# Kernel tuning notes

Measured on AMD Instinct MI355X. Metric: run time of the kernel, lower is better.

Reference implementation:

```python
import jax, jax.numpy as jnp
import numpy as np

BS, QLEN, KLEN = 2, 64, 64
N_HEADS, D_KV = 8, 64
INNER = N_HEADS * D_KV  # 512
VOCAB = 4096


def _layernorm(x, g, b, eps=1e-6):
    m = jnp.mean(x, axis=-1, keepdims=True)
    v = jnp.mean(jnp.square(x - m), axis=-1, keepdims=True)
    return (x - m) * jax.lax.rsqrt(v + eps) * g + b


def _l2norm(x, eps=1e-12):
    sq = jnp.sum(jnp.square(x), axis=-1, keepdims=True)
    return x * jax.lax.rsqrt(jnp.maximum(sq, eps))


def setup_inputs() -> dict:
    key = jax.random.key(0)
    ks = jax.random.split(key, 8)
    d = {
        'query': jax.random.normal(ks[0], (BS, QLEN, INNER), jnp.float32),
        'key': jax.random.normal(ks[1], (BS, KLEN, INNER), jnp.float32),
        'q_position_embeddings': jax.random.normal(ks[2], (BS, QLEN, INNER), jnp.float32),
        'k_position_embeddings': jax.random.normal(ks[3], (BS, KLEN, INNER), jnp.float32),
        'wi_w': jax.random.normal(ks[4], (2 * INNER, INNER), jnp.float32) / np.sqrt(2 * INNER),
        'vq_dict': jax.random.normal(ks[5], (VOCAB, D_KV), jnp.float32) * np.sqrt(2.0 / (VOCAB + D_KV)),
        'vq_ln_g': jnp.ones((D_KV,), jnp.float32),
        'vq_ln_b': jnp.zeros((D_KV,), jnp.float32),
        'vq_o_w': jax.random.normal(ks[6], (D_KV, D_KV), jnp.float32) / np.sqrt(D_KV),
        'ln_g': jnp.ones((D_KV,), jnp.float32),
        'ln_b': jnp.zeros((D_KV,), jnp.float32),
    }
    return d


def reference(query, key, q_position_embeddings, k_position_embeddings,
              wi_w, vq_dict, vq_ln_g, vq_ln_b, vq_o_w, ln_g, ln_b):
    bs, qlen, dim = query.shape
    klen = key.shape[1]

    q = query + q_position_embeddings
    k = key + k_position_embeddings
    # wi(concat([q, 0])) == q @ wi_w[:dim]; wi(concat([0, k])) == k @ wi_w[dim:]
    q_proj = jnp.einsum('bqd,de->bqe', q, wi_w[:dim])   # [bs, qlen, inner]
    k_proj = jnp.einsum('bkd,de->bke', k, wi_w[dim:])   # [bs, klen, inner]

    # pairwise outer sum -> [bs, qlen, klen, inner] -> tokens of size d_kv
    rcr = q_proj[:, :, None, :] + k_proj[:, None, :, :]
    y = rcr.reshape(bs, qlen * klen * N_HEADS, D_KV)

    # --- VectorQuantizer (eval mode: no dropout, loss = 0) ---
    y_n = _l2norm(y)
    d_n = _l2norm(vq_dict)
    sim = jnp.einsum('bnd,vd->bnv', y_n, d_n)           # [bs, N, vocab]
    word_idx = jnp.argmax(sim, axis=-1)                 # [bs, N] int
    word_sim = jnp.max(sim, axis=-1)                    # [bs, N]
    z = vq_dict[word_idx]                               # gather
    emb = jax.lax.stop_gradient(z - y) + y              # straight-through
    emb = _layernorm(emb, vq_ln_g, vq_ln_b)
    emb = jnp.einsum('bnd,de->bne', emb, vq_o_w)

    r3 = emb.reshape(bs, qlen, klen, N_HEADS, D_KV)
    r3_scores = word_sim.reshape(bs, qlen, klen, N_HEADS, 1)
    out_ids = word_idx.reshape(bs, qlen, klen, N_HEADS, 1)

    r3_weighted = jnp.mean(r3 * r3_scores, axis=2)      # [bs, qlen, n_heads, d_kv]
    r3_weighted = jnp.transpose(r3_weighted, (0, 2, 1, 3))  # [bs, n_heads, qlen, d_kv]
    r3_weighted = _layernorm(r3_weighted, ln_g, ln_b)
    return r3_weighted, out_ids, r3_scores
```

## Files before the change

kernel.cpp:

```cpp
#include <hip/hip_runtime.h>
#include <math.h>

#define BS 2
#define QLEN 64
#define KLEN 64
#define NH 8
#define DKV 64
#define INNER 512
#define VOCAB 4096
#define CHUNKV 64
#define RS 130
#define BUFD (CHUNKV * RS)

typedef double vdbl4 __attribute__((ext_vector_type(4)));
typedef double vdbl2 __attribute__((ext_vector_type(2)));


__global__ __launch_bounds__(256) void k_prep(
    const float* __restrict__ q_in, const float* __restrict__ k_in,
    const float* __restrict__ qpe, const float* __restrict__ kpe,
    const float* __restrict__ wi,
    const float* __restrict__ vq, const float* __restrict__ g,
    const float* __restrict__ bta, const float* __restrict__ ow,
    double* __restrict__ qp, double* __restrict__ kp,
    double* __restrict__ dnt, float* __restrict__ E,
    unsigned long long* __restrict__ bestf)
{
    __shared__ double S[1600];
    __shared__ float Osh[4096];
    int bid = blockIdx.x;
    int t = threadIdx.x;

    if (bid < 1024) {
        int side = bid >> 9;
        int b    = (bid >> 8) & 1;
        int rp   = (bid >> 3) & 31;
        int cb   = bid & 7;
        const float* xin = side ? k_in : q_in;
        const float* pin = side ? kpe : qpe;
        double* outp = side ? kp : qp;
        int wrow0 = side ? INNER : 0;
        int r0 = rp * 2;
        double* xs = S;
        double* red = S + 1024;
        for (int i = t; i < 2 * INNER; i += 256) {
            int rr = i >> 9, dd = i & 511;
            int gidx = (b * 64 + r0 + rr) * INNER + dd;
            xs[rr * INNER + dd] = (double)xin[gidx] + (double)pin[gidx];
        }
        __syncthreads();
        int col = cb * 64 + (t & 63);
        int dh = t >> 6;
        double a0 = 0.0, a1 = 0.0;
        #pragma unroll 8
        for (int d = dh * 128; d < dh * 128 + 128; ++d) {
            double w = (double)wi[(size_t)(wrow0 + d) * INNER + col];
            a0 = fma(xs[d], w, a0);
            a1 = fma(xs[INNER + d], w, a1);
        }
        red[(dh * 2 + 0) * 64 + (t & 63)] = a0;
        red[(dh * 2 + 1) * 64 + (t & 63)] = a1;
        __syncthreads();
        if (t < 128) {
            int rr = t >> 6, c2 = t & 63;
            double s = (red[(0 * 2 + rr) * 64 + c2] + red[(1 * 2 + rr) * 64 + c2])
                     + (red[(2 * 2 + rr) * 64 + c2] + red[(3 * 2 + rr) * 64 + c2]);
            outp[(size_t)(b * 64 + r0 + rr) * INNER + cb * 64 + c2] = s;
        }
    } else {
        int db = bid - 1024;
        if (db < 256) bestf[db * 256 + t] = 0ull;
        double* Lsh = S;
        double* Dsh = S + 256;
        int vb = db * 4;
        int wv = t >> 6, lane = t & 63;
        for (int i = t; i < 4096; i += 256) Osh[i] = ow[i];
        int v = vb + wv;
        double z = (double)vq[v * DKV + lane];
        double s2 = z * z, s1 = z;
        for (int m = 32; m >= 1; m >>= 1) { s2 += __shfl_xor(s2, m); s1 += __shfl_xor(s1, m); }
        Dsh[lane * 5 + wv] = z * (1.0 / sqrt(fmax(s2, 1e-12)));
        double mean = s1 * (1.0 / 64.0);
        double d0 = z - mean;
        double vv2 = d0 * d0;
        for (int m = 32; m >= 1; m >>= 1) vv2 += __shfl_xor(vv2, m);
        vv2 *= (1.0 / 64.0);
        Lsh[wv * 64 + lane] = d0 * (1.0 / sqrt(vv2 + 1e-6)) * (double)g[lane] + (double)bta[lane];
        __syncthreads();
        double c0 = 0.0, c1 = 0.0, c2 = 0.0, c3 = 0.0;
        #pragma unroll 4
        for (int gg = 0; gg < 16; ++gg) {
            int jj = gg * 4;
            c0 = fma(Lsh[wv * 64 + jj + 0], (double)Osh[(jj + 0) * 64 + lane], c0);
            c1 = fma(Lsh[wv * 64 + jj + 1], (double)Osh[(jj + 1) * 64 + lane], c1);
            c2 = fma(Lsh[wv * 64 + jj + 2], (double)Osh[(jj + 2) * 64 + lane], c2);
            c3 = fma(Lsh[wv * 64 + jj + 3], (double)Osh[(jj + 3) * 64 + lane], c3);
        }
        E[v * DKV + lane] = (float)((c0 + c1) + (c2 + c3));
        {
            int j = t >> 2, vloc = t & 3;
            dnt[(size_t)j * VOCAB + vb + vloc] = Dsh[j * 5 + vloc];
        }
    }
}

__global__ __launch_bounds__(1024, 4) void k_simscan(
    const double* __restrict__ qp, const double* __restrict__ kp,
    const double* __restrict__ dnt,
    unsigned long long* __restrict__ bestf)
{
    int bid = blockIdx.x;
    int bh = bid & 15, cg = bid >> 4;
    int b = bh >> 3, h = bh & 7;
    int t = threadIdx.x;
    int w = t >> 6, l = t & 63;

    __shared__ double S[2 * BUFD];

    int asub = l >> 4;
    int lrow = l & 15;
    bool isprod = (w < 8);

    int drow[4], dcol[4];
    {
        vdbl4 prow = (vdbl4){0.0, 0.0, 0.0, 0.0};
        vdbl4 pcol = (vdbl4){0.0, 0.0, 0.0, 0.0};
        double a_row = (asub == 0) ? (double)lrow : 0.0;
        double b_one = (asub == 0) ? 1.0 : 0.0;
        double a_one = (asub == 0) ? 1.0 : 0.0;
        double b_col = (asub == 0) ? (double)lrow : 0.0;
        prow = __builtin_amdgcn_mfma_f64_16x16x4f64(a_row, b_one, prow, 0, 0, 0);
        pcol = __builtin_amdgcn_mfma_f64_16x16x4f64(a_one, b_col, pcol, 0, 0, 0);
        #pragma unroll
        for (int r = 0; r < 4; ++r) { drow[r] = (int)prow[r]; dcol[r] = (int)pcol[r]; }
    }

    double afr[16];
    if (isprod) {
        const double* src = (w < 4) ? qp : kp;
        int arow = (w & 3) * 16 + lrow;
        #pragma unroll
        for (int ks = 0; ks < 16; ++ks)
            afr[ks] = src[(size_t)(b * 64 + arow) * INNER + h * 64 + ks * 4 + asub];
    }

    int ci = t - 512;
    int qg = ci & 15, kg = (ci >> 4) & 31;
    double best[4][2];
    #pragma unroll
    for (int i = 0; i < 4; ++i)
        #pragma unroll
        for (int j = 0; j < 2; ++j) best[i][j] = 0.0;

    for (int step = 0; step < 5; ++step) {
        if (isprod && step < 4) {
            int v0 = (cg * 4 + step) * CHUNKV;
            double* buf = S + (step & 1) * BUFD;
            vdbl4 acc[4];
            #pragma unroll
            for (int vt = 0; vt < 4; ++vt) acc[vt] = (vdbl4){0.0, 0.0, 0.0, 0.0};
            size_t base = (size_t)asub * VOCAB + v0 + lrow;
            double bcur[4], bnext[4];
            #pragma unroll
            for (int vt = 0; vt < 4; ++vt) bcur[vt] = dnt[base + vt * 16];
            #pragma unroll
            for (int ks = 0; ks < 16; ++ks) {
                if (ks < 15) {
                    size_t krow = base + (size_t)((ks + 1) * 4) * VOCAB;
                    #pragma unroll
                    for (int vt = 0; vt < 4; ++vt) bnext[vt] = dnt[krow + vt * 16];
                }
                #pragma unroll
                for (int vt = 0; vt < 4; ++vt)
                    acc[vt] = __builtin_amdgcn_mfma_f64_16x16x4f64(
                        afr[ks], bcur[vt], acc[vt], 0, 0, 0);
                if (ks < 15) {
                    #pragma unroll
                    for (int vt = 0; vt < 4; ++vt) bcur[vt] = bnext[vt];
                }
            }
            bool isq = (w < 4);
            #pragma unroll
            for (int vt = 0; vt < 4; ++vt)
                #pragma unroll
                for (int r = 0; r < 4; ++r) {
                    int vl = vt * 16 + dcol[r];
                    int grow = (w & 3) * 16 + drow[r];
                    int slot = isq ? ((grow & 15) * 4 + (grow >> 4))
                                   : (64 + (grow & 31) * 2 + (grow >> 5));
                    unsigned long long code =
                        (unsigned long long)((4095 - (v0 + vl)) << 1);
                    double s = fma(acc[vt][r], 1.0 / 64.0, 1.5);
                    unsigned long long bb2 = __double_as_longlong(s) & ~0x1FFFull;
                    if (isq) bb2 |= code;
                    buf[vl * RS + slot] = __longlong_as_double(bb2);
                }
        }
        if (!isprod && step >= 1) {
            double* buf = S + ((step - 1) & 1) * BUFD;
            #pragma unroll 2
            for (int v = 0; v < CHUNKV; ++v) {
                vdbl2 q01 = *(const vdbl2*)&buf[v * RS + qg * 4];
                vdbl2 q23 = *(const vdbl2*)&buf[v * RS + qg * 4 + 2];
                vdbl2 k01 = *(const vdbl2*)&buf[v * RS + 64 + kg * 2];
                best[0][0] = fmax(best[0][0], q01[0] + k01[0]);
                best[0][1] = fmax(best[0][1], q01[0] + k01[1]);
                best[1][0] = fmax(best[1][0], q01[1] + k01[0]);
                best[1][1] = fmax(best[1][1], q01[1] + k01[1]);
                best[2][0] = fmax(best[2][0], q23[0] + k01[0]);
                best[2][1] = fmax(best[2][1], q23[0] + k01[1]);
                best[3][0] = fmax(best[3][0], q23[1] + k01[0]);
                best[3][1] = fmax(best[3][1], q23[1] + k01[1]);
            }
        }
        if (step < 4) __syncthreads();
    }

    if (!isprod) {
        #pragma unroll
        for (int i = 0; i < 4; ++i)
            #pragma unroll
            for (int j = 0; j < 2; ++j) {
                int q = qg + 16 * i, k = kg + 32 * j;
                atomicMax(&bestf[((size_t)bh * 64 + q) * 64 + k],
                          (unsigned long long)__double_as_longlong(best[i][j]));
            }
    }
}

__global__ __launch_bounds__(256) void k_combine(
    const unsigned long long* __restrict__ bestf,
    const double* __restrict__ qp, const double* __restrict__ kp,
    const float* __restrict__ E,
    const float* __restrict__ lng, const float* __restrict__ lnb,
    float* __restrict__ out)
{
    int bid = blockIdx.x;
    int bh = bid >> 4, qg = bid & 15;
    int b = bh >> 3, h = bh & 7;
    int t = threadIdx.x;
    int w = t >> 6, lane = t & 63;
    int q0 = qg * 4;

    __shared__ double SC[4416];
    double* qs_l = SC;
    double* ks_l = SC + 256;
    __shared__ float ws_l[4][64];
    __shared__ int  idx_l[4][64];

    {
        int row = t >> 6, d = t & 63;
        qs_l[row * 64 + d] = qp[(size_t)(b * 64 + q0 + row) * INNER + h * 64 + d];
    }
    for (int i = t; i < 4096; i += 256) {
        int kr = i >> 6, d = i & 63;
        ks_l[kr * 65 + d] = kp[(size_t)(b * 64 + kr) * INNER + h * 64 + d];
    }
    __syncthreads();

    int qq = t >> 6;
    int k = t & 63;
    int q = q0 + qq;
    double gdot = 0.0, qn2 = 0.0, kn2 = 0.0;
    for (int d = 0; d < 64; ++d) {
        double xq = qs_l[qq * 64 + d];
        double xk = ks_l[k * 65 + d];
        gdot = fma(xq, xk, gdot);
        qn2 = fma(xq, xq, qn2);
        kn2 = fma(xk, xk, kn2);
    }

    unsigned long long bb = bestf[((size_t)bh * 64 + q) * 64 + k];
    int vidx = 4095 - (int)(bb & 0xFFFull);
    double sval = __longlong_as_double(bb & ~0x1FFFull);
    double tru = (sval - 3.0) * 64.0;
    double n2 = qn2 + kn2 + 2.0 * gdot;
    double wsim = tru * (1.0 / sqrt(fmax(n2, 1e-12)));

    size_t oidx = ((size_t)(b * QLEN + q) * KLEN + k) * NH + h;
    out[65536 + oidx] = (float)vidx;
    out[131072 + oidx] = (float)wsim;

    ws_l[w][k] = (float)wsim;
    idx_l[w][k] = vidx;
    __syncthreads();

    int d = lane;
    float acc = 0.0f;
    for (int k2 = 0; k2 < 64; ++k2)
        acc += E[idx_l[w][k2] * DKV + d] * ws_l[w][k2];
    acc *= (1.0f / 64.0f);
    float mean = acc;
    for (int m = 32; m >= 1; m >>= 1) mean += __shfl_xor(mean, m);
    mean *= (1.0f / 64.0f);
    float dv = acc - mean;
    float var = dv * dv;
    for (int m = 32; m >= 1; m >>= 1) var += __shfl_xor(var, m);
    var *= (1.0f / 64.0f);
    float o = dv * rsqrtf(var + 1e-6f) * lng[d] + lnb[d];
    out[(((size_t)b * NH + h) * QLEN + q) * DKV + d] = o;
}

extern "C" void kernel_launch(void* const* d_in, const int* in_sizes, int n_in,
                              void* d_out, int out_size, void* d_ws, size_t ws_size,
                              hipStream_t stream) {
    const float* query = (const float*)d_in[0];
    const float* key   = (const float*)d_in[1];
    const float* qpe   = (const float*)d_in[2];
    const float* kpe   = (const float*)d_in[3];
    const float* wi    = (const float*)d_in[4];
    const float* vq    = (const float*)d_in[5];
    const float* vqg   = (const float*)d_in[6];
    const float* vqb   = (const float*)d_in[7];
    const float* ow    = (const float*)d_in[8];
    const float* lng   = (const float*)d_in[9];
    const float* lnb   = (const float*)d_in[10];
    float* out = (float*)d_out;

    char* ws = (char*)d_ws;
    double* qp  = (double*)(ws + 0);
    double* kp  = (double*)(ws + 524288);
    double* dnt = (double*)(ws + 1048576);
    float*  E   = (float*) (ws + 3145728);
    unsigned long long* bestf = (unsigned long long*)(ws + 4194304);

    k_prep   <<<2048, 256, 0, stream>>>(query, key, qpe, kpe, wi, vq, vqg, vqb, ow,
                                        qp, kp, dnt, E, bestf);
    k_simscan<<<256, 1024, 0, stream>>>(qp, kp, dnt, bestf);
    k_combine<<<256, 256, 0, stream>>>(bestf, qp, kp, E, lng, lnb, out);
}
```

Before: 154.9 us.

## Halve simscan block size with 4x4 register tiles and smaller vocab chunks

Restructures the similarity-scan kernel into 512-thread blocks over 32-entry vocab chunks. Each of the four producer waves now computes 2x2 MFMA tiles, reusing each B fragment across two A row tiles. Each consumer thread keeps a 4x4 best tile, giving more reuse per shared-memory load. The grid doubles to 512 blocks to cover the vocabulary, which raises parallelism but also doubles the atomicMax traffic and the redundant A-fragment loads.

```diff
diff --git a/kernel.cpp b/kernel.cpp
--- a/kernel.cpp
+++ b/kernel.cpp
@@ -8,12 +8,11 @@
 #define DKV 64
 #define INNER 512
 #define VOCAB 4096
-#define CHUNKV 64
-#define RS 130
+#define CHUNKV 32
+#define RS 129
 #define BUFD (CHUNKV * RS)
 
 typedef double vdbl4 __attribute__((ext_vector_type(4)));
-typedef double vdbl2 __attribute__((ext_vector_type(2)));
 
 
 __global__ __launch_bounds__(256) void k_prep(
@@ -104,13 +103,13 @@
     }
 }
 
-__global__ __launch_bounds__(1024, 4) void k_simscan(
+__global__ __launch_bounds__(512, 4) void k_simscan(
     const double* __restrict__ qp, const double* __restrict__ kp,
     const double* __restrict__ dnt,
     unsigned long long* __restrict__ bestf)
 {
     int bid = blockIdx.x;
-    int bh = bid & 15, cg = bid >> 4;
+    int bh = bid & 15, vg = bid >> 4;
     int b = bh >> 3, h = bh & 7;
     int t = threadIdx.x;
     int w = t >> 6, l = t & 63;
@@ -119,7 +118,7 @@
 
     int asub = l >> 4;
     int lrow = l & 15;
-    bool isprod = (w < 8);
+    bool isprod = (w < 4);
 
     int drow[4], dcol[4];
     {
@@ -135,82 +134,89 @@
         for (int r = 0; r < 4; ++r) { drow[r] = (int)prow[r]; dcol[r] = (int)pcol[r]; }
     }
 
-    double afr[16];
+    double afr[2][16];
     if (isprod) {
-        const double* src = (w < 4) ? qp : kp;
-        int arow = (w & 3) * 16 + lrow;
+        const double* src = (w < 2) ? qp : kp;
+        int half = w & 1;
         #pragma unroll
-        for (int ks = 0; ks < 16; ++ks)
-            afr[ks] = src[(size_t)(b * 64 + arow) * INNER + h * 64 + ks * 4 + asub];
-    }
-
-    int ci = t - 512;
-    int qg = ci & 15, kg = (ci >> 4) & 31;
-    double best[4][2];
+        for (int rt = 0; rt < 2; ++rt) {
+            int arow = half * 32 + rt * 16 + lrow;
+            #pragma unroll
+            for (int ks = 0; ks < 16; ++ks)
+                afr[rt][ks] = src[(size_t)(b * 64 + arow) * INNER + h * 64 + ks * 4 + asub];
+        }
+    }
+
+    int ci = t - 256;
+    int qg = ci & 15, kg = (ci >> 4) & 15;
+    double best[4][4];
     #pragma unroll
     for (int i = 0; i < 4; ++i)
         #pragma unroll
-        for (int j = 0; j < 2; ++j) best[i][j] = 0.0;
+        for (int j = 0; j < 4; ++j) best[i][j] = 0.0;
 
     for (int step = 0; step < 5; ++step) {
         if (isprod && step < 4) {
-            int v0 = (cg * 4 + step) * CHUNKV;
+            int v0 = (vg * 4 + step) * CHUNKV;
             double* buf = S + (step & 1) * BUFD;
-            vdbl4 acc[4];
-            #pragma unroll
-            for (int vt = 0; vt < 4; ++vt) acc[vt] = (vdbl4){0.0, 0.0, 0.0, 0.0};
+            vdbl4 acc[2][2];
+            #pragma unroll
+            for (int rt = 0; rt < 2; ++rt)
+                #pragma unroll
+                for (int vt = 0; vt < 2; ++vt) acc[rt][vt] = (vdbl4){0.0, 0.0, 0.0, 0.0};
             size_t base = (size_t)asub * VOCAB + v0 + lrow;
-            double bcur[4], bnext[4];
-            #pragma unroll
-            for (int vt = 0; vt < 4; ++vt) bcur[vt] = dnt[base + vt * 16];
+            double bcur[2], bnext[2];
+            #pragma unroll
+            for (int vt = 0; vt < 2; ++vt) bcur[vt] = dnt[base + vt * 16];
             #pragma unroll
             for (int ks = 0; ks < 16; ++ks) {
                 if (ks < 15) {
                     size_t krow = base + (size_t)((ks + 1) * 4) * VOCAB;
                     #pragma unroll
-                    for (int vt = 0; vt < 4; ++vt) bnext[vt] = dnt[krow + vt * 16];
+                    for (int vt = 0; vt < 2; ++vt) bnext[vt] = dnt[krow + vt * 16];
                 }
                 #pragma unroll
-                for (int vt = 0; vt < 4; ++vt)
-                    acc[vt] = __builtin_amdgcn_mfma_f64_16x16x4f64(
-                        afr[ks], bcur[vt], acc[vt], 0, 0, 0);
+                for (int rt = 0; rt < 2; ++rt)
+                    #pragma unroll
+                    for (int vt = 0; vt < 2; ++vt)
+                        acc[rt][vt] = __builtin_amdgcn_mfma_f64_16x16x4f64(
+                            afr[rt][ks], bcur[vt], acc[rt][vt], 0, 0, 0);
                 if (ks < 15) {
                     #pragma unroll
-                    for (int vt = 0; vt < 4; ++vt) bcur[vt] = bnext[vt];
+                    for (int vt = 0; vt < 2; ++vt) bcur[vt] = bnext[vt];
                 }
             }
-            bool isq = (w < 4);
-            #pragma unroll
-            for (int vt = 0; vt < 4; ++vt)
-                #pragma unroll
-                for (int r = 0; r < 4; ++r) {
-                    int vl = vt * 16 + dcol[r];
-                    int grow = (w & 3) * 16 + drow[r];
-                    int slot = isq ? ((grow & 15) * 4 + (grow >> 4))
-                                   : (64 + (grow & 31) * 2 + (grow >> 5));
-                    unsigned long long code =
-                        (unsigned long long)((4095 - (v0 + vl)) << 1);
-                    double s = fma(acc[vt][r], 1.0 / 64.0, 1.5);
-                    unsigned long long bb2 = __double_as_longlong(s) & ~0x1FFFull;
-                    if (isq) bb2 |= code;
-                    buf[vl * RS + slot] = __longlong_as_double(bb2);
-                }
+            bool isq = (w < 2);
+            int rb0 = (isq ? 0 : 64) + (w & 1) * 32;
+            #pragma unroll
+            for (int rt = 0; rt < 2; ++rt)
+                #pragma unroll
+                for (int vt = 0; vt < 2; ++vt)
+                    #pragma unroll
+                    for (int r = 0; r < 4; ++r) {
+                        int vl = vt * 16 + dcol[r];
+                        unsigned long long code =
+                            (unsigned long long)((4095 - (v0 + vl)) << 1);
+                        double s = fma(acc[rt][vt][r], 1.0 / 64.0, 1.5);
+                        unsigned long long bb2 = __double_as_longlong(s) & ~0x1FFFull;
+                        if (isq) bb2 |= code;
+                        buf[vl * RS + rb0 + rt * 16 + drow[r]] = __longlong_as_double(bb2);
+                    }
         }
         if (!isprod && step >= 1) {
             double* buf = S + ((step - 1) & 1) * BUFD;
             #pragma unroll 2
             for (int v = 0; v < CHUNKV; ++v) {
-                vdbl2 q01 = *(const vdbl2*)&buf[v * RS + qg * 4];
-                vdbl2 q23 = *(const vdbl2*)&buf[v * RS + qg * 4 + 2];
-                vdbl2 k01 = *(const vdbl2*)&buf[v * RS + 64 + kg * 2];
-                best[0][0] = fmax(best[0][0], q01[0] + k01[0]);
-                best[0][1] = fmax(best[0][1], q01[0] + k01[1]);
-                best[1][0] = fmax(best[1][0], q01[1] + k01[0]);
-                best[1][1] = fmax(best[1][1], q01[1] + k01[1]);
-                best[2][0] = fmax(best[2][0], q23[0] + k01[0]);
-                best[2][1] = fmax(best[2][1], q23[0] + k01[1]);
-                best[3][0] = fmax(best[3][0], q23[1] + k01[0]);
-                best[3][1] = fmax(best[3][1], q23[1] + k01[1]);
+                double qv[4], kv[4];
+                #pragma unroll
+                for (int i = 0; i < 4; ++i) qv[i] = buf[v * RS + qg + 16 * i];
+                #pragma unroll
+                for (int j = 0; j < 4; ++j) kv[j] = buf[v * RS + 64 + kg + 16 * j];
+                #pragma unroll
+                for (int i = 0; i < 4; ++i)
+                    #pragma unroll
+                    for (int j = 0; j < 4; ++j)
+                        best[i][j] = fmax(best[i][j], qv[i] + kv[j]);
             }
         }
         if (step < 4) __syncthreads();
@@ -220,8 +226,8 @@
         #pragma unroll
         for (int i = 0; i < 4; ++i)
             #pragma unroll
-            for (int j = 0; j < 2; ++j) {
-                int q = qg + 16 * i, k = kg + 32 * j;
+            for (int j = 0; j < 4; ++j) {
+                int q = qg + 16 * i, k = kg + 16 * j;
                 atomicMax(&bestf[((size_t)bh * 64 + q) * 64 + k],
                           (unsigned long long)__double_as_longlong(best[i][j]));
             }
@@ -326,6 +332,6 @@
 
     k_prep   <<<2048, 256, 0, stream>>>(query, key, qpe, kpe, wi, vq, vqg, vqb, ow,
                                         qp, kp, dnt, E, bestf);
-    k_simscan<<<256, 1024, 0, stream>>>(qp, kp, dnt, bestf);
+    k_simscan<<<512, 512, 0, stream>>>(qp, kp, dnt, bestf);
     k_combine<<<256, 256, 0, stream>>>(bestf, qp, kp, E, lng, lnb, out);
 }
```

After: 169.2 us. 9.3% more time.

## Split combine kernel per query row with four-way reductions across waves

Applied to the files above, without the earlier changes.

The combine kernel now runs one block per (batch, head, query) instead of per four queries, giving 1024 blocks instead of 256. The 64-dim dot products and norms, and the weighted embedding gather, are split across four waves into partial sums that are reduced in shared memory. This removes the 64x64 key tile staging in LDS and shortens the serial per-thread loops. In exchange, the key rows are reread from global memory by every query block, and the extra barriers leave three of four waves idle during the final stages.

```diff
diff --git a/kernel.cpp b/kernel.cpp
--- a/kernel.cpp
+++ b/kernel.cpp
@@ -236,69 +236,84 @@
     float* __restrict__ out)
 {
     int bid = blockIdx.x;
-    int bh = bid >> 4, qg = bid & 15;
+    int bh = bid & 15, q = bid >> 4;
     int b = bh >> 3, h = bh & 7;
     int t = threadIdx.x;
     int w = t >> 6, lane = t & 63;
-    int q0 = qg * 4;
-
-    __shared__ double SC[4416];
-    double* qs_l = SC;
-    double* ks_l = SC + 256;
-    __shared__ float ws_l[4][64];
-    __shared__ int  idx_l[4][64];
+
+    __shared__ double qrow[64];
+    __shared__ double gpart[4][64];
+    __shared__ double knpart[4][64];
+    __shared__ double qnpart[4];
+    __shared__ float  ws_l[64];
+    __shared__ int    idx_l[64];
+    __shared__ float  epart[4][64];
+
+    if (t < 64) qrow[t] = qp[(size_t)(b * 64 + q) * INNER + h * 64 + t];
+    __syncthreads();
 
     {
-        int row = t >> 6, d = t & 63;
-        qs_l[row * 64 + d] = qp[(size_t)(b * 64 + q0 + row) * INNER + h * 64 + d];
-    }
-    for (int i = t; i < 4096; i += 256) {
-        int kr = i >> 6, d = i & 63;
-        ks_l[kr * 65 + d] = kp[(size_t)(b * 64 + kr) * INNER + h * 64 + d];
+        const double* krow = kp + (size_t)(b * 64 + lane) * INNER + h * 64 + w * 16;
+        double gd = 0.0, kn = 0.0;
+        #pragma unroll
+        for (int i = 0; i < 16; ++i) {
+            double xk = krow[i];
+            gd = fma(qrow[w * 16 + i], xk, gd);
+            kn = fma(xk, xk, kn);
+        }
+        gpart[w][lane] = gd;
+        knpart[w][lane] = kn;
+        if (lane == 0) {
+            double qn = 0.0;
+            #pragma unroll
+            for (int i = 0; i < 16; ++i) { double xq = qrow[w * 16 + i]; qn = fma(xq, xq, qn); }
+            qnpart[w] = qn;
+        }
     }
     __syncthreads();
 
-    int qq = t >> 6;
-    int k = t & 63;
-    int q = q0 + qq;
-    double gdot = 0.0, qn2 = 0.0, kn2 = 0.0;
-    for (int d = 0; d < 64; ++d) {
-        double xq = qs_l[qq * 64 + d];
-        double xk = ks_l[k * 65 + d];
-        gdot = fma(xq, xk, gdot);
-        qn2 = fma(xq, xq, qn2);
-        kn2 = fma(xk, xk, kn2);
-    }
-
-    unsigned long long bb = bestf[((size_t)bh * 64 + q) * 64 + k];
-    int vidx = 4095 - (int)(bb & 0xFFFull);
-    double sval = __longlong_as_double(bb & ~0x1FFFull);
-    double tru = (sval - 3.0) * 64.0;
-    double n2 = qn2 + kn2 + 2.0 * gdot;
-    double wsim = tru * (1.0 / sqrt(fmax(n2, 1e-12)));
-
-    size_t oidx = ((size_t)(b * QLEN + q) * KLEN + k) * NH + h;
-    out[65536 + oidx] = (float)vidx;
-    out[131072 + oidx] = (float)wsim;
-
-    ws_l[w][k] = (float)wsim;
-    idx_l[w][k] = vidx;
+    if (w == 0) {
+        int k = lane;
+        double gdot = (gpart[0][k] + gpart[1][k]) + (gpart[2][k] + gpart[3][k]);
+        double kn2  = (knpart[0][k] + knpart[1][k]) + (knpart[2][k] + knpart[3][k]);
+        double qn2  = (qnpart[0] + qnpart[1]) + (qnpart[2] + qnpart[3]);
+        unsigned long long bb = bestf[((size_t)bh * 64 + q) * 64 + k];
+        int vidx = 4095 - (int)(bb & 0xFFFull);
+        double sval = __longlong_as_double(bb & ~0x1FFFull);
+        double tru = (sval - 3.0) * 64.0;
+        double n2 = qn2 + kn2 + 2.0 * gdot;
+        double wsim = tru * (1.0 / sqrt(fmax(n2, 1e-12)));
+        size_t oidx = ((size_t)(b * QLEN + q) * KLEN + k) * NH + h;
+        out[65536 + oidx] = (float)vidx;
+        out[131072 + oidx] = (float)wsim;
+        ws_l[k] = (float)wsim;
+        idx_l[k] = vidx;
+    }
     __syncthreads();
 
-    int d = lane;
-    float acc = 0.0f;
-    for (int k2 = 0; k2 < 64; ++k2)
-        acc += E[idx_l[w][k2] * DKV + d] * ws_l[w][k2];
-    acc *= (1.0f / 64.0f);
-    float mean = acc;
-    for (int m = 32; m >= 1; m >>= 1) mean += __shfl_xor(mean, m);
-    mean *= (1.0f / 64.0f);
-    float dv = acc - mean;
-    float var = dv * dv;
-    for (int m = 32; m >= 1; m >>= 1) var += __shfl_xor(var, m);
-    var *= (1.0f / 64.0f);
-    float o = dv * rsqrtf(var + 1e-6f) * lng[d] + lnb[d];
-    out[(((size_t)b * NH + h) * QLEN + q) * DKV + d] = o;
+    {
+        int d = lane;
+        float acc = 0.0f;
+        #pragma unroll 4
+        for (int k2 = w * 16; k2 < w * 16 + 16; ++k2)
+            acc += E[idx_l[k2] * DKV + d] * ws_l[k2];
+        epart[w][d] = acc;
+    }
+    __syncthreads();
+
+    if (w == 0) {
+        int d = lane;
+        float acc = ((epart[0][d] + epart[1][d]) + (epart[2][d] + epart[3][d])) * (1.0f / 64.0f);
+        float mean = acc;
+        for (int m = 32; m >= 1; m >>= 1) mean += __shfl_xor(mean, m);
+        mean *= (1.0f / 64.0f);
+        float dv = acc - mean;
+        float var = dv * dv;
+        for (int m = 32; m >= 1; m >>= 1) var += __shfl_xor(var, m);
+        var *= (1.0f / 64.0f);
+        float o = dv * rsqrtf(var + 1e-6f) * lng[d] + lnb[d];
+        out[(((size_t)b * NH + h) * QLEN + q) * DKV + d] = o;
+    }
 }
 
 extern "C" void kernel_launch(void* const* d_in, const int* in_sizes, int n_in,
@@ -327,5 +342,5 @@
     k_prep   <<<2048, 256, 0, stream>>>(query, key, qpe, kpe, wi, vq, vqg, vqb, ow,
                                         qp, kp, dnt, E, bestf);
     k_simscan<<<256, 1024, 0, stream>>>(qp, kp, dnt, bestf);
-    k_combine<<<256, 256, 0, stream>>>(bestf, qp, kp, E, lng, lnb, out);
+    k_combine<<<1024, 256, 0, stream>>>(bestf, qp, kp, E, lng, lnb, out);
 }
```

Measured after the change: 154.2 us. Within noise of the previous version (-0.4%).

## Fuse combine stage into simscan via last-block-per-head completion counter

Applied to the files above, without the earlier changes.

Removes the separate combine kernel launch and folds its work into k_simscan. Each (batch, head) group keeps an atomic counter, and the last of its 16 blocks to finish runs the combine work (norms, weights, gather-weighted mean, layernorm) for all 64 queries. This drops one kernel launch and the gap between kernels. In exchange, the combine for each head now runs on a single block of 16 instead of 16 parallel blocks, so the tail work is more serialized.

```diff
diff --git a/kernel.cpp b/kernel.cpp
--- a/kernel.cpp
+++ b/kernel.cpp
@@ -24,7 +24,7 @@
     const float* __restrict__ bta, const float* __restrict__ ow,
     double* __restrict__ qp, double* __restrict__ kp,
     double* __restrict__ dnt, float* __restrict__ E,
-    unsigned long long* __restrict__ bestf)
+    unsigned long long* __restrict__ bestf, int* __restrict__ bhcnt)
 {
     __shared__ double S[1600];
     __shared__ float Osh[4096];
@@ -70,6 +70,7 @@
     } else {
         int db = bid - 1024;
         if (db < 256) bestf[db * 256 + t] = 0ull;
+        if (db == 0 && t < 16) bhcnt[t] = 0;
         double* Lsh = S;
         double* Dsh = S + 256;
         int vb = db * 4;
@@ -107,7 +108,10 @@
 __global__ __launch_bounds__(1024, 4) void k_simscan(
     const double* __restrict__ qp, const double* __restrict__ kp,
     const double* __restrict__ dnt,
-    unsigned long long* __restrict__ bestf)
+    unsigned long long* __restrict__ bestf, int* __restrict__ bhcnt,
+    const float* __restrict__ E,
+    const float* __restrict__ lng, const float* __restrict__ lnb,
+    float* __restrict__ out)
 {
     int bid = blockIdx.x;
     int bh = bid & 15, cg = bid >> 4;
@@ -116,6 +120,7 @@
     int w = t >> 6, l = t & 63;
 
     __shared__ double S[2 * BUFD];
+    __shared__ int lastdone;
 
     int asub = l >> 4;
     int lrow = l & 15;
@@ -226,79 +231,74 @@
                           (unsigned long long)__double_as_longlong(best[i][j]));
             }
     }
-}
-
-__global__ __launch_bounds__(256) void k_combine(
-    const unsigned long long* __restrict__ bestf,
-    const double* __restrict__ qp, const double* __restrict__ kp,
-    const float* __restrict__ E,
-    const float* __restrict__ lng, const float* __restrict__ lnb,
-    float* __restrict__ out)
-{
-    int bid = blockIdx.x;
-    int bh = bid >> 4, qg = bid & 15;
-    int b = bh >> 3, h = bh & 7;
-    int t = threadIdx.x;
-    int w = t >> 6, lane = t & 63;
-    int q0 = qg * 4;
-
-    __shared__ double SC[4416];
-    double* qs_l = SC;
-    double* ks_l = SC + 256;
-    __shared__ float ws_l[4][64];
-    __shared__ int  idx_l[4][64];
-
-    {
-        int row = t >> 6, d = t & 63;
-        qs_l[row * 64 + d] = qp[(size_t)(b * 64 + q0 + row) * INNER + h * 64 + d];
-    }
-    for (int i = t; i < 4096; i += 256) {
-        int kr = i >> 6, d = i & 63;
-        ks_l[kr * 65 + d] = kp[(size_t)(b * 64 + kr) * INNER + h * 64 + d];
-    }
-    __syncthreads();
-
-    int qq = t >> 6;
-    int k = t & 63;
-    int q = q0 + qq;
-    double gdot = 0.0, qn2 = 0.0, kn2 = 0.0;
-    for (int d = 0; d < 64; ++d) {
-        double xq = qs_l[qq * 64 + d];
-        double xk = ks_l[k * 65 + d];
-        gdot = fma(xq, xk, gdot);
-        qn2 = fma(xq, xq, qn2);
-        kn2 = fma(xk, xk, kn2);
-    }
-
-    unsigned long long bb = bestf[((size_t)bh * 64 + q) * 64 + k];
-    int vidx = 4095 - (int)(bb & 0xFFFull);
-    double sval = __longlong_as_double(bb & ~0x1FFFull);
-    double tru = (sval - 3.0) * 64.0;
-    double n2 = qn2 + kn2 + 2.0 * gdot;
-    double wsim = tru * (1.0 / sqrt(fmax(n2, 1e-12)));
-
-    size_t oidx = ((size_t)(b * QLEN + q) * KLEN + k) * NH + h;
-    out[65536 + oidx] = (float)vidx;
-    out[131072 + oidx] = (float)wsim;
-
-    ws_l[w][k] = (float)wsim;
-    idx_l[w][k] = vidx;
-    __syncthreads();
-
-    int d = lane;
-    float acc = 0.0f;
-    for (int k2 = 0; k2 < 64; ++k2)
-        acc += E[idx_l[w][k2] * DKV + d] * ws_l[w][k2];
-    acc *= (1.0f / 64.0f);
-    float mean = acc;
-    for (int m = 32; m >= 1; m >>= 1) mean += __shfl_xor(mean, m);
-    mean *= (1.0f / 64.0f);
-    float dv = acc - mean;
-    float var = dv * dv;
-    for (int m = 32; m >= 1; m >>= 1) var += __shfl_xor(var, m);
-    var *= (1.0f / 64.0f);
-    float o = dv * rsqrtf(var + 1e-6f) * lng[d] + lnb[d];
-    out[(((size_t)b * NH + h) * QLEN + q) * DKV + d] = o;
+
+    __syncthreads();
+    __threadfence();
+    if (t == 0) lastdone = (atomicAdd(&bhcnt[bh], 1) == 15);
+    __syncthreads();
+    if (!lastdone) return;
+
+    double* qs_l = S;
+    double* ks_l = S + 4160;
+    float*  ws_l  = (float*)(S + 8320);
+    int*    idx_l = (int*)(S + 8320 + 2048);
+    double* qn_l  = S + 8320 + 4096;
+    double* kn_l  = S + 8320 + 4160;
+
+    for (int i = t; i < 8192; i += 1024) {
+        int row = i >> 6, d = i & 63;
+        if (row < 64) qs_l[row * 65 + d] = qp[(size_t)(b * 64 + row) * INNER + h * 64 + d];
+        else ks_l[(row - 64) * 65 + d] = kp[(size_t)(b * 64 + row - 64) * INNER + h * 64 + d];
+    }
+    __syncthreads();
+    if (t < 128) {
+        int r = t & 63;
+        const double* src = (t < 64) ? (qs_l + r * 65) : (ks_l + r * 65);
+        double s = 0.0;
+        for (int d = 0; d < 64; ++d) s = fma(src[d], src[d], s);
+        if (t < 64) qn_l[r] = s; else kn_l[r] = s;
+    }
+    __syncthreads();
+
+    #pragma unroll
+    for (int i = 0; i < 4; ++i) {
+        int p = t + i * 1024;
+        int q = p >> 6, k = p & 63;
+        double gd = 0.0;
+        for (int d = 0; d < 64; ++d) gd = fma(qs_l[q * 65 + d], ks_l[k * 65 + d], gd);
+        unsigned long long bb = atomicMax(&bestf[((size_t)bh * 64 + q) * 64 + k], 0ull);
+        int vidx = 4095 - (int)(bb & 0xFFFull);
+        double sval = __longlong_as_double(bb & ~0x1FFFull);
+        double tru = (sval - 3.0) * 64.0;
+        double n2 = qn_l[q] + kn_l[k] + 2.0 * gd;
+        double wsim = tru * (1.0 / sqrt(fmax(n2, 1e-12)));
+        size_t oidx = ((size_t)(b * QLEN + q) * KLEN + k) * NH + h;
+        out[65536 + oidx] = (float)vidx;
+        out[131072 + oidx] = (float)wsim;
+        ws_l[q * 64 + k] = (float)wsim;
+        idx_l[q * 64 + k] = vidx;
+    }
+    __syncthreads();
+
+    #pragma unroll
+    for (int i = 0; i < 4; ++i) {
+        int item = t + i * 1024;
+        int q = item >> 6, d = item & 63;
+        float acc = 0.0f;
+        #pragma unroll 4
+        for (int k2 = 0; k2 < 64; ++k2)
+            acc += E[idx_l[q * 64 + k2] * DKV + d] * ws_l[q * 64 + k2];
+        acc *= (1.0f / 64.0f);
+        float mean = acc;
+        for (int m = 32; m >= 1; m >>= 1) mean += __shfl_xor(mean, m);
+        mean *= (1.0f / 64.0f);
+        float dv = acc - mean;
+        float var = dv * dv;
+        for (int m = 32; m >= 1; m >>= 1) var += __shfl_xor(var, m);
+        var *= (1.0f / 64.0f);
+        float o = dv * rsqrtf(var + 1e-6f) * lng[d] + lnb[d];
+        out[(((size_t)b * NH + h) * QLEN + q) * DKV + d] = o;
+    }
 }
 
 extern "C" void kernel_launch(void* const* d_in, const int* in_sizes, int n_in,
@@ -323,9 +323,9 @@
     double* dnt = (double*)(ws + 1048576);
     float*  E   = (float*) (ws + 3145728);
     unsigned long long* bestf = (unsigned long long*)(ws + 4194304);
+    int* bhcnt = (int*)(ws + 4718592);
 
     k_prep   <<<2048, 256, 0, stream>>>(query, key, qpe, kpe, wi, vq, vqg, vqb, ow,
-                                        qp, kp, dnt, E, bestf);
-    k_simscan<<<256, 1024, 0, stream>>>(qp, kp, dnt, bestf);
-    k_combine<<<256, 256, 0, stream>>>(bestf, qp, kp, E, lng, lnb, out);
+                                        qp, kp, dnt, E, bestf, bhcnt);
+    k_simscan<<<256, 1024, 0, stream>>>(qp, kp, dnt, bestf, bhcnt, E, lng, lnb, out);
 }
```

Result: slower. 265.0 us (+71.1%).
